# Kernel tuning notes

Hardware: AMD Instinct MI355X
Metric: run time of the kernel (lower is better)

## Reference

```python
import jax, jax.numpy as jnp
import numpy as np

B, N, D = 4, 4096, 3
Q = jnp.array([0.05, 0.95, 0.25, 0.75], dtype=jnp.float32)  # q_begin + q_end


def _nn_diff(S1, S2):
    # For each point in S1 find nearest point in S2 (squared L2), return S1 - closest_S2.
    # d2: [N, N] built via the ||a||^2 + ||b||^2 - 2ab expansion (avoids [N,N,D]).
    d2 = (jnp.sum(S1 * S1, axis=-1, keepdims=True)
          + jnp.sum(S2 * S2, axis=-1)[None, :]
          - 2.0 * (S1 @ S2.T))
    idx = jnp.argmin(d2, axis=1)          # [N] nearest index in S2
    return S1 - S2[idx]                   # [N, D] vector residuals (mean=False path)


def _masked_std(v, mask):
    # torch.std over the masked subset (unbiased, correction=1), mask is float {0,1}.
    n = jnp.sum(mask)
    mean = jnp.sum(v * mask) / n
    var = jnp.sum(mask * (v - mean) ** 2) / (n - 1.0)
    return jnp.sqrt(var)


def _mask_std_pair(d):
    # mask_by_Z: quantiles computed under no_grad (stop_gradient), then std of each subset.
    v = d.reshape(-1)
    q = jnp.quantile(jax.lax.stop_gradient(v), Q.astype(v.dtype))
    mask_begin = ((v < q[0]) | (v > q[1])).astype(v.dtype)
    mask_end = ((v > q[2]) & (v < q[3])).astype(v.dtype)
    return _masked_std(v, mask_begin), _masked_std(v, mask_end)


def _sigma_distance(S1, S2):
    d12 = _nn_diff(S1, S2)  # S1 -> S2 residuals
    d21 = _nn_diff(S2, S1)  # S2 -> S1 residuals
    b1, e1 = _mask_std_pair(d12)
    b2, e2 = _mask_std_pair(d21)
    return jnp.maximum(b1, b2), jnp.maximum(e1, e2)


def setup_inputs() -> dict:
    key = jax.random.key(0)
    kx, ky = jax.random.split(key)
    x = jax.random.normal(kx, (B, N, D), dtype=jnp.float32)
    y = jax.random.normal(ky, (B, N, D), dtype=jnp.float32)
    return {"x": x, "y": y}


def reference(x, y):
    begin, end = jax.vmap(_sigma_distance)(x, y)  # [B], [B]
    return begin.mean(), end.mean()
```

## Files before the change

### kernel.cpp

```cpp
#include <hip/hip_runtime.h>
#include <math.h>

constexpr int B_  = 4;
constexpr int N_  = 4096;
constexpr int NV  = N_ * 3;
constexpr int NCCH = 16;
constexpr int CCH  = N_ / NCCH;
constexpr int TPB_TAIL = 1024;

__device__ inline unsigned f2k(float f) {
    unsigned b = __float_as_uint(f);
    return b ^ ((unsigned)((int)b >> 31) | 0x80000000u);
}
__device__ inline float k2f(unsigned k) {
    unsigned b = (k & 0x80000000u) ? (k ^ 0x80000000u) : ~k;
    return __uint_as_float(b);
}

__global__ __launch_bounds__(256) void prescale_kernel(const float* __restrict__ x,
                                                       const float* __restrict__ y,
                                                       float4* __restrict__ preX,
                                                       float4* __restrict__ preY) {
    const int t = blockIdx.x * 256 + threadIdx.x;
    const float* src = blockIdx.y == 0 ? x : y;
    float4* dst      = blockIdx.y == 0 ? preX : preY;
    float bx = src[t * 3 + 0];
    float by = src[t * 3 + 1];
    float bz = src[t * 3 + 2];
    dst[t] = make_float4(-2.f * bx, -2.f * by, -2.f * bz,
                         bx * bx + by * by + bz * bz);
}

__global__ __launch_bounds__(256) void nn_scalar_kernel(const float* __restrict__ x,
                                                        const float* __restrict__ y,
                                                        const float4* __restrict__ preX,
                                                        const float4* __restrict__ preY,
                                                        float2* __restrict__ part) {
    const int pair = blockIdx.z;
    const int b    = pair >> 1;
    const int dir  = pair & 1;
    const float*  S1 = (dir == 0 ? x : y) + b * NV;
    const float4* P2 = (dir == 0 ? preY : preX) + b * N_;
    const int cbase = blockIdx.x * CCH;

    const int q = blockIdx.y * 256 + threadIdx.x;
    const float ax = S1[q * 3 + 0];
    const float ay = S1[q * 3 + 1];
    const float az = S1[q * 3 + 2];

    float bd = INFINITY;
    int idx = 0;
    #pragma unroll 16
    for (int j = 0; j < CCH; ++j) {
        const float4 c = P2[cbase + j];
        float d2 = fmaf(ax, c.x, fmaf(ay, c.y, fmaf(az, c.z, c.w)));
        if (d2 < bd) idx = cbase + j;
        bd = fminf(d2, bd);
    }
    part[(size_t)(pair * NCCH + blockIdx.x) * N_ + q] = make_float2(bd, (float)idx);
}

__global__ __launch_bounds__(256) void merge_keys_kernel(const float* __restrict__ x,
                                                         const float* __restrict__ y,
                                                         const float2* __restrict__ part,
                                                         unsigned* __restrict__ keys) {
    const int pair = blockIdx.y;
    const int b    = pair >> 1;
    const int dir  = pair & 1;
    const float* S1 = (dir == 0 ? x : y) + b * NV;
    const float* S2 = (dir == 0 ? y : x) + b * NV;
    const int q = blockIdx.x * 256 + threadIdx.x;

    float best = INFINITY;
    int bidx = 0;
    #pragma unroll
    for (int c = 0; c < NCCH; ++c) {
        float2 p = part[(size_t)(pair * NCCH + c) * N_ + q];
        if (p.x < best) { best = p.x; bidx = (int)p.y; }
    }
    unsigned* kp = keys + (size_t)pair * NV;
    kp[0 * N_ + q] = f2k(S1[q * 3 + 0] - S2[bidx * 3 + 0]);
    kp[1 * N_ + q] = f2k(S1[q * 3 + 1] - S2[bidx * 3 + 1]);
    kp[2 * N_ + q] = f2k(S1[q * 3 + 2] - S2[bidx * 3 + 2]);
}

__global__ __launch_bounds__(TPB_TAIL) void tail_kernel(const unsigned* __restrict__ gkeys,
                                                        float* __restrict__ stats) {
    __shared__ unsigned keys[NV];
    __shared__ int hist8[8][256];
    __shared__ unsigned s_prefix[4];
    __shared__ int s_want[4];
    __shared__ int s_cnt[4];
    __shared__ unsigned s_mn[4];
    __shared__ float s_qv[4];
    __shared__ float red[64];
    __shared__ float sh[8];

    const int pair = blockIdx.x;
    const int tid  = threadIdx.x;
    const int lane = tid & 63;
    const int wid  = tid >> 6;

    const uint4* g4 = (const uint4*)(gkeys + (size_t)pair * NV);
    uint4* l4w = (uint4*)keys;
    #pragma unroll
    for (int i = 0; i < 3; ++i)
        l4w[i * TPB_TAIL + tid] = g4[i * TPB_TAIL + tid];
    if (tid < 4) {
        const float Qs[4] = {0.05f, 0.95f, 0.25f, 0.75f};
        s_prefix[tid] = 0u;
        s_want[tid]   = (int)floorf(Qs[tid] * (float)(NV - 1));
    }
    __syncthreads();

    const uint4* k4 = (const uint4*)keys;
    #pragma unroll 1
    for (int pass = 0; pass < 4; ++pass) {
        const int shift = 24 - 8 * pass;
        ((int*)hist8)[tid]             = 0;
        ((int*)hist8)[tid + TPB_TAIL]  = 0;
        __syncthreads();

        if (pass == 0) {
            int* h = hist8[wid & 7];
            for (int i = tid; i < NV / 4; i += TPB_TAIL) {
                uint4 kv = k4[i];
                atomicAdd(&h[kv.x >> 24], 1);
                atomicAdd(&h[kv.y >> 24], 1);
                atomicAdd(&h[kv.z >> 24], 1);
                atomicAdd(&h[kv.w >> 24], 1);
            }
        } else {
            const unsigned pmask = 0xFFFFFFFFu << (32 - 8 * pass);
            const unsigned pf0 = s_prefix[0], pf1 = s_prefix[1];
            const unsigned pf2 = s_prefix[2], pf3 = s_prefix[3];
            for (int i = tid; i < NV / 4; i += TPB_TAIL) {
                uint4 kv = k4[i];
                const unsigned ks[4] = {kv.x, kv.y, kv.z, kv.w};
                #pragma unroll
                for (int u = 0; u < 4; ++u) {
                    const unsigned k  = ks[u];
                    const unsigned kp = k & pmask;
                    const int bin = (int)((k >> shift) & 255u);
                    if (kp == pf0) atomicAdd(&hist8[0][bin], 1);
                    if (kp == pf1) atomicAdd(&hist8[1][bin], 1);
                    if (kp == pf2) atomicAdd(&hist8[2][bin], 1);
                    if (kp == pf3) atomicAdd(&hist8[3][bin], 1);
                }
            }
        }
        __syncthreads();

        if (wid < 4) {
            int c0 = 0, c1 = 0, c2 = 0, c3 = 0;
            if (pass == 0) {
                #pragma unroll
                for (int cp = 0; cp < 8; ++cp) {
                    c0 += hist8[cp][lane * 4 + 0]; c1 += hist8[cp][lane * 4 + 1];
                    c2 += hist8[cp][lane * 4 + 2]; c3 += hist8[cp][lane * 4 + 3];
                }
            } else {
                c0 = hist8[wid][lane * 4 + 0]; c1 = hist8[wid][lane * 4 + 1];
                c2 = hist8[wid][lane * 4 + 2]; c3 = hist8[wid][lane * 4 + 3];
            }
            const int want = s_want[wid];
            int s = c0 + c1 + c2 + c3;
            int pre = s;
            #pragma unroll
            for (int off = 1; off < 64; off <<= 1) {
                int u = __shfl_up(pre, off);
                if (lane >= off) pre += u;
            }
            const int excl = pre - s;
            const bool hit = (want >= excl) && (want < excl + s);
            unsigned long long m = __ballot(hit);
            const int hl = (int)(__ffsll(m) - 1);
            if (lane == hl) {
                int w = want - excl;
                int sel;
                if      (w < c0)           { sel = lane * 4 + 0; }
                else if (w < c0 + c1)      { sel = lane * 4 + 1; w -= c0; }
                else if (w < c0 + c1 + c2) { sel = lane * 4 + 2; w -= c0 + c1; }
                else                       { sel = lane * 4 + 3; w -= c0 + c1 + c2; }
                s_prefix[wid] |= ((unsigned)sel) << shift;
                s_want[wid] = w;
            }
        }
        __syncthreads();
    }

    if (tid < 4) { s_cnt[tid] = 0; s_mn[tid] = 0xFFFFFFFFu; }
    __syncthreads();
    const unsigned kq0 = s_prefix[0], kq1 = s_prefix[1];
    const unsigned kq2 = s_prefix[2], kq3 = s_prefix[3];
    int cnt0 = 0, cnt1 = 0, cnt2 = 0, cnt3 = 0;
    unsigned mn0 = 0xFFFFFFFFu, mn1 = 0xFFFFFFFFu, mn2 = 0xFFFFFFFFu, mn3 = 0xFFFFFFFFu;
    for (int i = tid; i < NV / 4; i += TPB_TAIL) {
        uint4 kv = k4[i];
        const unsigned ks[4] = {kv.x, kv.y, kv.z, kv.w};
        #pragma unroll
        for (int u = 0; u < 4; ++u) {
            const unsigned k = ks[u];
            if (k <= kq0) cnt0++; else if (k < mn0) mn0 = k;
            if (k <= kq1) cnt1++; else if (k < mn1) mn1 = k;
            if (k <= kq2) cnt2++; else if (k < mn2) mn2 = k;
            if (k <= kq3) cnt3++; else if (k < mn3) mn3 = k;
        }
    }
    #pragma unroll
    for (int off = 32; off > 0; off >>= 1) {
        cnt0 += __shfl_down(cnt0, off); cnt1 += __shfl_down(cnt1, off);
        cnt2 += __shfl_down(cnt2, off); cnt3 += __shfl_down(cnt3, off);
        unsigned u0 = __shfl_down(mn0, off); mn0 = u0 < mn0 ? u0 : mn0;
        unsigned u1 = __shfl_down(mn1, off); mn1 = u1 < mn1 ? u1 : mn1;
        unsigned u2 = __shfl_down(mn2, off); mn2 = u2 < mn2 ? u2 : mn2;
        unsigned u3 = __shfl_down(mn3, off); mn3 = u3 < mn3 ? u3 : mn3;
    }
    if (lane == 0) {
        atomicAdd(&s_cnt[0], cnt0); atomicMin(&s_mn[0], mn0);
        atomicAdd(&s_cnt[1], cnt1); atomicMin(&s_mn[1], mn1);
        atomicAdd(&s_cnt[2], cnt2); atomicMin(&s_mn[2], mn2);
        atomicAdd(&s_cnt[3], cnt3); atomicMin(&s_mn[3], mn3);
    }
    __syncthreads();
    if (tid < 4) {
        const float Qs[4] = {0.05f, 0.95f, 0.25f, 0.75f};
        const float pos = Qs[tid] * (float)(NV - 1);
        const int   k0  = (int)floorf(pos);
        const float fr  = pos - (float)k0;
        const float v0  = k2f(s_prefix[tid]);
        const float v1  = (s_cnt[tid] >= k0 + 2) ? v0 : k2f(s_mn[tid]);
        s_qv[tid] = v0 + fr * (v1 - v0);
    }
    __syncthreads();
    const float q0 = s_qv[0], q1 = s_qv[1], q2 = s_qv[2], q3 = s_qv[3];

    float cb = 0.f, sb = 0.f, ce = 0.f, se = 0.f;
    for (int i = tid; i < NV / 4; i += TPB_TAIL) {
        uint4 kv = k4[i];
        const unsigned ks[4] = {kv.x, kv.y, kv.z, kv.w};
        #pragma unroll
        for (int u = 0; u < 4; ++u) {
            const float val = k2f(ks[u]);
            if ((val < q0) || (val > q1)) { cb += 1.f; sb += val; }
            if ((val > q2) && (val < q3)) { ce += 1.f; se += val; }
        }
    }
    #pragma unroll
    for (int off = 32; off > 0; off >>= 1) {
        cb += __shfl_down(cb, off); sb += __shfl_down(sb, off);
        ce += __shfl_down(ce, off); se += __shfl_down(se, off);
    }
    if (lane == 0) {
        red[wid * 4 + 0] = cb; red[wid * 4 + 1] = sb;
        red[wid * 4 + 2] = ce; red[wid * 4 + 3] = se;
    }
    __syncthreads();
    if (tid == 0) {
        float tcb = 0.f, tsb = 0.f, tce = 0.f, tse = 0.f;
        for (int w = 0; w < 16; ++w) {
            tcb += red[w * 4 + 0]; tsb += red[w * 4 + 1];
            tce += red[w * 4 + 2]; tse += red[w * 4 + 3];
        }
        sh[0] = tsb / tcb;  sh[1] = tse / tce;
        sh[2] = tcb;        sh[3] = tce;
    }
    __syncthreads();
    const float mean_b = sh[0], mean_e = sh[1];
    const float nb = sh[2], ne = sh[3];

    float vb = 0.f, ve = 0.f;
    for (int i = tid; i < NV / 4; i += TPB_TAIL) {
        uint4 kv = k4[i];
        const unsigned ks[4] = {kv.x, kv.y, kv.z, kv.w};
        #pragma unroll
        for (int u = 0; u < 4; ++u) {
            const float val = k2f(ks[u]);
            if ((val < q0) || (val > q1)) { float d = val - mean_b; vb += d * d; }
            if ((val > q2) && (val < q3)) { float d = val - mean_e; ve += d * d; }
        }
    }
    #pragma unroll
    for (int off = 32; off > 0; off >>= 1) {
        vb += __shfl_down(vb, off);
        ve += __shfl_down(ve, off);
    }
    __syncthreads();
    if (lane == 0) { red[wid * 2 + 0] = vb; red[wid * 2 + 1] = ve; }
    __syncthreads();
    if (tid == 0) {
        float tvb = 0.f, tve = 0.f;
        for (int w = 0; w < 16; ++w) { tvb += red[w * 2 + 0]; tve += red[w * 2 + 1]; }
        stats[pair * 2 + 0] = sqrtf(tvb / (nb - 1.f));
        stats[pair * 2 + 1] = sqrtf(tve / (ne - 1.f));
    }
}

__global__ void final_kernel(const float* __restrict__ stats, float* __restrict__ out) {
    if (threadIdx.x == 0 && blockIdx.x == 0) {
        float sb = 0.f, se = 0.f;
        for (int b = 0; b < B_; ++b) {
            float b1 = stats[(b * 2 + 0) * 2 + 0];
            float b2 = stats[(b * 2 + 1) * 2 + 0];
            float e1 = stats[(b * 2 + 0) * 2 + 1];
            float e2 = stats[(b * 2 + 1) * 2 + 1];
            sb += fmaxf(b1, b2);
            se += fmaxf(e1, e2);
        }
        out[0] = sb / (float)B_;
        out[1] = se / (float)B_;
    }
}

extern "C" void kernel_launch(void* const* d_in, const int* in_sizes, int n_in,
                              void* d_out, int out_size, void* d_ws, size_t ws_size,
                              hipStream_t stream) {
    const float* x = (const float*)d_in[0];
    const float* y = (const float*)d_in[1];
    float* out = (float*)d_out;

    unsigned* keys  = (unsigned*)d_ws;
    float*    stats = (float*)(keys + (size_t)8 * NV);
    float4*   preX  = (float4*)(stats + 16);
    float4*   preY  = preX + (size_t)B_ * N_;
    float2*   part  = (float2*)(preY + (size_t)B_ * N_);

    prescale_kernel<<<dim3(B_ * N_ / 256, 2), 256, 0, stream>>>(x, y, preX, preY);
    nn_scalar_kernel<<<dim3(NCCH, N_ / 256, 8), 256, 0, stream>>>(x, y, preX, preY, part);
    merge_keys_kernel<<<dim3(N_ / 256, 8), 256, 0, stream>>>(x, y, part, keys);
    tail_kernel<<<8, TPB_TAIL, 0, stream>>>(keys, stats);
    final_kernel<<<1, 64, 0, stream>>>(stats, out);
}
```

Baseline: 65.65 us.

## Fuse NN merge into tail kernel and compute two queries per thread

Removes the separate merge kernel by folding the partial-argmin reduction and residual-key computation into the tail kernel, writing keys straight into shared memory instead of staging them in global memory. The NN kernel now processes two query points per thread, reusing each candidate load, and splits candidates into 32 chunks instead of 16 to keep the grid size the same. The trade-off is that the merge work now runs on only 8 blocks inside the tail kernel, with twice as many partial results to reduce, so that phase gets far less parallelism.

After: 123.6 us. +88.3%, slower.

```diff
diff --git a/kernel.cpp b/kernel.cpp
--- a/kernel.cpp
+++ b/kernel.cpp
@@ -4,8 +4,9 @@
 constexpr int B_  = 4;
 constexpr int N_  = 4096;
 constexpr int NV  = N_ * 3;
-constexpr int NCCH = 16;
+constexpr int NCCH = 32;
 constexpr int CCH  = N_ / NCCH;
+constexpr int QPT  = 2;
 constexpr int TPB_TAIL = 1024;
 
 __device__ inline unsigned f2k(float f) {
@@ -35,7 +36,7 @@
                                                         const float* __restrict__ y,
                                                         const float4* __restrict__ preX,
                                                         const float4* __restrict__ preY,
-                                                        float2* __restrict__ part) {
+                                                        float4* __restrict__ part) {
     const int pair = blockIdx.z;
     const int b    = pair >> 1;
     const int dir  = pair & 1;
@@ -43,49 +44,34 @@
     const float4* P2 = (dir == 0 ? preY : preX) + b * N_;
     const int cbase = blockIdx.x * CCH;
 
-    const int q = blockIdx.y * 256 + threadIdx.x;
-    const float ax = S1[q * 3 + 0];
-    const float ay = S1[q * 3 + 1];
-    const float az = S1[q * 3 + 2];
-
-    float bd = INFINITY;
-    int idx = 0;
-    #pragma unroll 16
+    const int q0 = blockIdx.y * 512 + threadIdx.x * QPT;
+    const float2* p2 = (const float2*)(S1 + q0 * 3);
+    const float2 v0 = p2[0], v1 = p2[1], v2 = p2[2];
+    const float ax0 = v0.x, ay0 = v0.y, az0 = v1.x;
+    const float ax1 = v1.y, ay1 = v2.x, az1 = v2.y;
+
+    float bd0 = INFINITY, bd1 = INFINITY;
+    int idx0 = 0, idx1 = 0;
+    #pragma unroll 8
     for (int j = 0; j < CCH; ++j) {
         const float4 c = P2[cbase + j];
-        float d2 = fmaf(ax, c.x, fmaf(ay, c.y, fmaf(az, c.z, c.w)));
-        if (d2 < bd) idx = cbase + j;
-        bd = fminf(d2, bd);
-    }
-    part[(size_t)(pair * NCCH + blockIdx.x) * N_ + q] = make_float2(bd, (float)idx);
-}
-
-__global__ __launch_bounds__(256) void merge_keys_kernel(const float* __restrict__ x,
-                                                         const float* __restrict__ y,
-                                                         const float2* __restrict__ part,
-                                                         unsigned* __restrict__ keys) {
-    const int pair = blockIdx.y;
-    const int b    = pair >> 1;
-    const int dir  = pair & 1;
-    const float* S1 = (dir == 0 ? x : y) + b * NV;
-    const float* S2 = (dir == 0 ? y : x) + b * NV;
-    const int q = blockIdx.x * 256 + threadIdx.x;
-
-    float best = INFINITY;
-    int bidx = 0;
-    #pragma unroll
-    for (int c = 0; c < NCCH; ++c) {
-        float2 p = part[(size_t)(pair * NCCH + c) * N_ + q];
-        if (p.x < best) { best = p.x; bidx = (int)p.y; }
-    }
-    unsigned* kp = keys + (size_t)pair * NV;
-    kp[0 * N_ + q] = f2k(S1[q * 3 + 0] - S2[bidx * 3 + 0]);
-    kp[1 * N_ + q] = f2k(S1[q * 3 + 1] - S2[bidx * 3 + 1]);
-    kp[2 * N_ + q] = f2k(S1[q * 3 + 2] - S2[bidx * 3 + 2]);
-}
-
-__global__ __launch_bounds__(TPB_TAIL) void tail_kernel(const unsigned* __restrict__ gkeys,
-                                                        float* __restrict__ stats) {
+        const int jg = cbase + j;
+        float d20 = fmaf(ax0, c.x, fmaf(ay0, c.y, fmaf(az0, c.z, c.w)));
+        float d21 = fmaf(ax1, c.x, fmaf(ay1, c.y, fmaf(az1, c.z, c.w)));
+        if (d20 < bd0) idx0 = jg;
+        bd0 = fminf(d20, bd0);
+        if (d21 < bd1) idx1 = jg;
+        bd1 = fminf(d21, bd1);
+    }
+
+    part[((size_t)(pair * NCCH + blockIdx.x) * N_ + q0) >> 1] =
+        make_float4(bd0, (float)idx0, bd1, (float)idx1);
+}
+
+__global__ __launch_bounds__(TPB_TAIL) void fused_tail_kernel(const float* __restrict__ x,
+                                                              const float* __restrict__ y,
+                                                              const float2* __restrict__ part,
+                                                              float* __restrict__ stats) {
     __shared__ unsigned keys[NV];
     __shared__ int hist8[8][256];
     __shared__ unsigned s_prefix[4];
@@ -100,12 +86,24 @@
     const int tid  = threadIdx.x;
     const int lane = tid & 63;
     const int wid  = tid >> 6;
-
-    const uint4* g4 = (const uint4*)(gkeys + (size_t)pair * NV);
-    uint4* l4w = (uint4*)keys;
+    const int b    = pair >> 1;
+    const int dir  = pair & 1;
+    const float* S1 = (dir == 0 ? x : y) + b * NV;
+    const float* S2 = (dir == 0 ? y : x) + b * NV;
+
     #pragma unroll
-    for (int i = 0; i < 3; ++i)
-        l4w[i * TPB_TAIL + tid] = g4[i * TPB_TAIL + tid];
+    for (int step = 0; step < 4; ++step) {
+        const int q = step * 1024 + tid;
+        float best = INFINITY; int bidx = 0;
+        #pragma unroll 8
+        for (int c = 0; c < NCCH; ++c) {
+            float2 p = part[(size_t)(pair * NCCH + c) * N_ + q];
+            if (p.x < best) { best = p.x; bidx = (int)p.y; }
+        }
+        keys[q * 3 + 0] = f2k(S1[q * 3 + 0] - S2[bidx * 3 + 0]);
+        keys[q * 3 + 1] = f2k(S1[q * 3 + 1] - S2[bidx * 3 + 1]);
+        keys[q * 3 + 2] = f2k(S1[q * 3 + 2] - S2[bidx * 3 + 2]);
+    }
     if (tid < 4) {
         const float Qs[4] = {0.05f, 0.95f, 0.25f, 0.75f};
         s_prefix[tid] = 0u;
@@ -319,15 +317,13 @@
     const float* y = (const float*)d_in[1];
     float* out = (float*)d_out;
 
-    unsigned* keys  = (unsigned*)d_ws;
-    float*    stats = (float*)(keys + (size_t)8 * NV);
-    float4*   preX  = (float4*)(stats + 16);
-    float4*   preY  = preX + (size_t)B_ * N_;
-    float2*   part  = (float2*)(preY + (size_t)B_ * N_);
+    float*  stats = (float*)d_ws;
+    float4* preX  = (float4*)(stats + 16);
+    float4* preY  = preX + (size_t)B_ * N_;
+    float4* part  = preY + (size_t)B_ * N_;
 
     prescale_kernel<<<dim3(B_ * N_ / 256, 2), 256, 0, stream>>>(x, y, preX, preY);
-    nn_scalar_kernel<<<dim3(NCCH, N_ / 256, 8), 256, 0, stream>>>(x, y, preX, preY, part);
-    merge_keys_kernel<<<dim3(N_ / 256, 8), 256, 0, stream>>>(x, y, part, keys);
-    tail_kernel<<<8, TPB_TAIL, 0, stream>>>(keys, stats);
+    nn_scalar_kernel<<<dim3(NCCH, N_ / 512, 8), 256, 0, stream>>>(x, y, preX, preY, part);
+    fused_tail_kernel<<<8, TPB_TAIL, 0, stream>>>(x, y, (const float2*)part, stats);
     final_kernel<<<1, 64, 0, stream>>>(stats, out);
 }
```
